# Kernel optimization log

Measured on AMD Instinct MI355X. Metric: run time of the kernel, lower is better.

The kernel has to match this reference:

```python
import jax, jax.numpy as jnp
import numpy as np
import math

THETA_BASE = 10000.0
RMS_EPS = 1.1920929e-07  # torch.finfo(float32).eps (nn.RMSNorm default eps=None)


def _rmsnorm(x, w):
    var = jnp.mean(x * x, axis=-1, keepdims=True)
    return x * jax.lax.rsqrt(var + RMS_EPS) * w


def _apply_pope(x, positions, pope_delta_raw, is_query):
    # x: (T, dk) pre-activation content -> magnitude via softplus
    dk = x.shape[-1]
    mu = jax.nn.softplus(x)
    freqs = THETA_BASE ** (jnp.arange(dk, dtype=jnp.float32) / dk)
    phi = positions[:, None] * freqs[None, :]  # (T, dk)
    if not is_query:
        phi = phi + (-2.0 * math.pi) * jax.nn.sigmoid(pope_delta_raw)
    return jnp.concatenate([mu * jnp.cos(phi), mu * jnp.sin(phi)], axis=-1)  # (T, 2*dk)


def setup_inputs() -> dict:
    key = jax.random.key(0)
    T, d, dk, dv = 8192, 1024, 64, 64
    dk_pope = 2 * dk
    ks = jax.random.split(key, 16)
    s = 0.02
    inp = {
        "x_seq": jax.random.normal(ks[0], (T, d), dtype=jnp.float32),
        "W_q": jax.random.normal(ks[1], (dk, d), dtype=jnp.float32) * s,
        "W_k": jax.random.normal(ks[2], (dk, d), dtype=jnp.float32) * s,
        "W_v": jax.random.normal(ks[3], (dv, d), dtype=jnp.float32) * s,
        "pope_delta_raw": jnp.zeros((dk,), dtype=jnp.float32),
        "W_alpha1": jax.random.normal(ks[4], (2 * dk, d), dtype=jnp.float32) * s,
        "W_alpha2": jax.random.normal(ks[5], (dk_pope, 2 * dk), dtype=jnp.float32) * s,
        "W_beta": jax.random.normal(ks[6], (1, d), dtype=jnp.float32) * s,
        "post_norm_w": jnp.ones((dv,), dtype=jnp.float32),
        "out_gate_W": jax.random.normal(ks[7], (dv, d), dtype=jnp.float32) * s,
        "W_out_W": jax.random.normal(ks[8], (d, dv), dtype=jnp.float32) * s,
        "ffn_norm_w": jnp.ones((d,), dtype=jnp.float32),
        "ffn_gate_W": jax.random.normal(ks[9], (d, d), dtype=jnp.float32) * s,
        "ffn_up_W": jax.random.normal(ks[10], (d, d), dtype=jnp.float32) * s,
        "ffn_down_W": jax.random.normal(ks[11], (d, d), dtype=jnp.float32) * s,
    }
    return inp


def reference(x_seq, W_q, W_k, W_v, pope_delta_raw, W_alpha1, W_alpha2, W_beta,
              post_norm_w, out_gate_W, W_out_W, ffn_norm_w, ffn_gate_W, ffn_up_W,
              ffn_down_W):
    T, d = x_seq.shape
    dk = W_q.shape[0]
    dk_pope = 2 * dk
    dv = W_v.shape[0]
    positions = jnp.arange(T, dtype=jnp.float32)

    q = _apply_pope(x_seq @ W_q.T, positions, pope_delta_raw, is_query=True)   # (T, dk_pope)
    k = _apply_pope(x_seq @ W_k.T, positions, pope_delta_raw, is_query=False)  # (T, dk_pope)
    v = jax.nn.silu(x_seq @ W_v.T)                                             # (T, dv)
    alpha = jax.nn.sigmoid(jax.nn.silu(x_seq @ W_alpha1.T) @ W_alpha2.T)       # (T, dk_pope)
    beta = jax.nn.sigmoid(x_seq @ W_beta.T)                                    # (T, 1)

    def step(S, inp):
        qt, kt, vt, at, bt = inp
        aS = at[:, None] * S                       # Diag(alpha) S, (dk_pope, dv)
        ktaS = kt @ aS                              # (dv,)
        S_new = aS + bt * kt[:, None] * (vt[None, :] - ktaS[None, :])
        ot = S_new.T @ qt                           # (dv,)
        return S_new, ot

    S0 = jnp.zeros((dk_pope, dv), dtype=x_seq.dtype)
    _, out = jax.lax.scan(step, S0, (q, k, v, alpha, beta))  # out: (T, dv)

    out = _rmsnorm(out, post_norm_w)
    out = out * jax.nn.sigmoid(x_seq @ out_gate_W.T)
    x = x_seq + out @ W_out_W.T
    h = _rmsnorm(x, ffn_norm_w)
    x = x + (jax.nn.silu(h @ ffn_gate_W.T) * (h @ ffn_up_W.T)) @ ffn_down_W.T
    return x
```

## Files before the change

### kernel.cpp

```cpp
#include <hip/hip_runtime.h>
#include <math.h>

#define T_SEQ 8192
#define D_MODEL 1024
#define DK 64
#define DKP 128
#define DV 64
#define C1LD 512
#define RMS_EPS 1.1920929e-07f
#define CHUNK 128
#define NCHUNK 64

typedef __attribute__((ext_vector_type(8))) __bf16 bf16x8;
typedef __attribute__((ext_vector_type(4))) float f32x4;

__device__ __forceinline__ float wave_sum(float x) {
#pragma unroll
  for (int off = 1; off < 64; off <<= 1) x += __shfl_xor(x, off, 64);
  return x;
}

template <int CTRL>
__device__ __forceinline__ float dpp_add(float x) {
  return x + __int_as_float(
                 __builtin_amdgcn_update_dpp(0, __float_as_int(x), CTRL, 0xF, 0xF, false));
}
__device__ __forceinline__ float sum16(float x) {
  x = dpp_add<0x121>(x);
  x = dpp_add<0x122>(x);
  x = dpp_add<0x124>(x);
  x = dpp_add<0x128>(x);
  return x;
}

__device__ __forceinline__ float sigmoidf_(float x) { return 1.0f / (1.0f + expf(-x)); }
__device__ __forceinline__ float siluf_(float x) { return x / (1.0f + expf(-x)); }

__device__ __forceinline__ unsigned short f2bf(float f) {
  unsigned u = __float_as_uint(f);
  u += 0x7fff + ((u >> 16) & 1);
  return (unsigned short)(u >> 16);
}

__global__ void init_tables(const float* __restrict__ delta, float* __restrict__ freq,
                            float* __restrict__ shift) {
  int i = threadIdx.x;
  freq[i] = (float)pow(10000.0, (double)i / 64.0);
  float s = 1.0f / (1.0f + expf(-delta[i]));
  shift[i] = -6.2831855f * s;
}

__global__ void build_wcat16(const float* __restrict__ Wq, const float* __restrict__ Wk,
                             const float* __restrict__ Wv, const float* __restrict__ Wa1,
                             const float* __restrict__ Wb, const float* __restrict__ Wg,
                             unsigned short* __restrict__ W16) {
  int idx = blockIdx.x * 256 + threadIdx.x;
  if (idx >= 512 * 1024) return;
  int row = idx >> 10, col = idx & 1023;
  float v = 0.f;
  if (row < 64) v = Wq[row * 1024 + col];
  else if (row < 128) v = Wk[(row - 64) * 1024 + col];
  else if (row < 192) v = Wv[(row - 128) * 1024 + col];
  else if (row < 320) v = Wa1[(row - 192) * 1024 + col];
  else if (row == 320) v = Wb[col];
  else if (row < 385) v = Wg[(row - 321) * 1024 + col];
  W16[idx] = f2bf(v);
}

__global__ void conv_bf16(const float* __restrict__ in, unsigned short* __restrict__ out,
                          int n4) {
  int i = blockIdx.x * 256 + threadIdx.x;
  if (i >= n4) return;
  float4 v = ((const float4*)in)[i];
  uint2 o;
  o.x = (unsigned)f2bf(v.x) | ((unsigned)f2bf(v.y) << 16);
  o.y = (unsigned)f2bf(v.z) | ((unsigned)f2bf(v.w) << 16);
  ((uint2*)out)[i] = o;
}

__global__ void conv_weights(const float* __restrict__ Wg, const float* __restrict__ Wu,
                             const float* __restrict__ Wd, const float* __restrict__ Wo,
                             unsigned short* __restrict__ Wg16, unsigned short* __restrict__ Wu16,
                             unsigned short* __restrict__ Wd16, unsigned short* __restrict__ Wo16) {
  int i = blockIdx.x * 256 + threadIdx.x;
  const float* src;
  unsigned short* dst;
  int base;
  if (i < 262144) { src = Wg; dst = Wg16; base = i; }
  else if (i < 524288) { src = Wu; dst = Wu16; base = i - 262144; }
  else if (i < 786432) { src = Wd; dst = Wd16; base = i - 524288; }
  else if (i < 802816) { src = Wo; dst = Wo16; base = i - 786432; }
  else return;
  float4 v = ((const float4*)src)[base];
  uint2 o;
  o.x = (unsigned)f2bf(v.x) | ((unsigned)f2bf(v.y) << 16);
  o.y = (unsigned)f2bf(v.z) | ((unsigned)f2bf(v.w) << 16);
  ((uint2*)dst)[base] = o;
}

__global__ __launch_bounds__(256) void gemm_bf16(const unsigned short* __restrict__ A,
                                                 const unsigned short* __restrict__ B,
                                                 const float* __restrict__ add,
                                                 float* __restrict__ C,
                                                 int M, int N, int K, int act) {
  __shared__ unsigned short As[128 * 32];
  __shared__ unsigned short Bs[128 * 32];
  const int tid = threadIdx.x;
  const int tm0 = blockIdx.x * 128, tn0 = blockIdx.y * 128;
  const int lane = tid & 63;
  const int w = tid >> 6;
  const int wr = (w >> 1) * 64, wc = (w & 1) * 64;
  const int fr = lane & 15, fq = lane >> 4;
  const int seg = w << 5;
  const int srow = lane >> 2;
  const int skc = (lane & 3) * 8;
  f32x4 acc[4][4];
#pragma unroll
  for (int a = 0; a < 4; ++a)
#pragma unroll
    for (int b = 0; b < 4; ++b) acc[a][b] = (f32x4){0.f, 0.f, 0.f, 0.f};

  for (int k0 = 0; k0 < K; k0 += 32) {
    __syncthreads();
#pragma unroll
    for (int j = 0; j < 2; ++j) {
      int r = seg + j * 16 + srow;
      __builtin_amdgcn_global_load_lds(
          (const __attribute__((address_space(1))) unsigned int*)(A + (size_t)(tm0 + r) * K + k0 + skc),
          (__attribute__((address_space(3))) unsigned int*)(As + (seg + j * 16) * 32),
          16, 0, 0);
      __builtin_amdgcn_global_load_lds(
          (const __attribute__((address_space(1))) unsigned int*)(B + (size_t)(tn0 + r) * K + k0 + skc),
          (__attribute__((address_space(3))) unsigned int*)(Bs + (seg + j * 16) * 32),
          16, 0, 0);
    }
    __syncthreads();
    bf16x8 af[4], bfr[4];
#pragma unroll
    for (int a = 0; a < 4; ++a)
      af[a] = *(const bf16x8*)(As + (wr + a * 16 + fr) * 32 + fq * 8);
#pragma unroll
    for (int b = 0; b < 4; ++b)
      bfr[b] = *(const bf16x8*)(Bs + (wc + b * 16 + fr) * 32 + fq * 8);
#pragma unroll
    for (int a = 0; a < 4; ++a)
#pragma unroll
      for (int b = 0; b < 4; ++b)
        acc[a][b] = __builtin_amdgcn_mfma_f32_16x16x32_bf16(af[a], bfr[b], acc[a][b], 0, 0, 0);
  }
#pragma unroll
  for (int a = 0; a < 4; ++a) {
#pragma unroll
    for (int b = 0; b < 4; ++b) {
#pragma unroll
      for (int r = 0; r < 4; ++r) {
        int row = tm0 + wr + a * 16 + fq * 4 + r;
        int col = tn0 + wc + b * 16 + fr;
        float v = acc[a][b][r];
        if (add) v += add[(size_t)row * N + col];
        if (act == 2) v = v / (1.0f + expf(-v));
        C[(size_t)row * N + col] = v;
      }
    }
  }
}

__global__ __launch_bounds__(256) void gemm_f32(const float* __restrict__ A,
                                                const float* __restrict__ B,
                                                const float* __restrict__ add,
                                                float* __restrict__ C,
                                                int M, int N, int K, int act) {
  __shared__ float As[16][68];
  __shared__ float Bs[16][68];
  const int bm = blockIdx.x * 64;
  const int bn = blockIdx.y * 64;
  const int tid = threadIdx.x;
  const int tm = tid >> 4, tn = tid & 15;
  const int lk = (tid & 3) << 2, lm = tid >> 2;
  float acc[4][4] = {{0.f}};
  const int ar = bm + lm;
  const int br = bn + lm;
  for (int k0 = 0; k0 < K; k0 += 16) {
    float4 a4 = make_float4(0.f, 0.f, 0.f, 0.f);
    float4 b4 = make_float4(0.f, 0.f, 0.f, 0.f);
    if (ar < M) a4 = *(const float4*)(A + (size_t)ar * K + k0 + lk);
    if (br < N) b4 = *(const float4*)(B + (size_t)br * K + k0 + lk);
    __syncthreads();
    As[lk][lm] = a4.x; As[lk + 1][lm] = a4.y; As[lk + 2][lm] = a4.z; As[lk + 3][lm] = a4.w;
    Bs[lk][lm] = b4.x; Bs[lk + 1][lm] = b4.y; Bs[lk + 2][lm] = b4.z; Bs[lk + 3][lm] = b4.w;
    __syncthreads();
#pragma unroll
    for (int kk = 0; kk < 16; ++kk) {
      float4 av = *(const float4*)&As[kk][tm << 2];
      float4 bv = *(const float4*)&Bs[kk][tn << 2];
      float a_[4] = {av.x, av.y, av.z, av.w};
      float b_[4] = {bv.x, bv.y, bv.z, bv.w};
#pragma unroll
      for (int i = 0; i < 4; ++i)
#pragma unroll
        for (int j = 0; j < 4; ++j) acc[i][j] = fmaf(a_[i], b_[j], acc[i][j]);
    }
  }
#pragma unroll
  for (int i = 0; i < 4; ++i) {
    int row = bm + (tm << 2) + i;
    if (row >= M) continue;
#pragma unroll
    for (int j = 0; j < 4; ++j) {
      int col = bn + (tn << 2) + j;
      if (col >= N) continue;
      float r = acc[i][j];
      if (add) r += add[(size_t)row * N + col];
      if (act == 1) r = 1.0f / (1.0f + expf(-r));
      else if (act == 2) r = r / (1.0f + expf(-r));
      C[(size_t)row * N + col] = r;
    }
  }
}

__global__ void act_split(const float* __restrict__ C1, float* __restrict__ vb,
                          float* __restrict__ a1s, float* __restrict__ betab) {
  int idx = blockIdx.x * 256 + threadIdx.x;
  if (idx >= T_SEQ * 193) return;
  int t = idx / 193, j = idx % 193;
  if (j < 64) {
    float x = C1[(size_t)t * C1LD + 128 + j];
    vb[(size_t)t * DV + j] = siluf_(x);
  } else if (j < 192) {
    float x = C1[(size_t)t * C1LD + 192 + (j - 64)];
    a1s[(size_t)t * DKP + (j - 64)] = siluf_(x);
  } else {
    betab[t] = sigmoidf_(C1[(size_t)t * C1LD + 320]);
  }
}

__global__ __launch_bounds__(256) void pope_kernel(const float* __restrict__ C1,
                                                   const float* __restrict__ freq,
                                                   const float* __restrict__ shift,
                                                   float* __restrict__ qb, float* __restrict__ kb) {
  int idx = blockIdx.x * 256 + threadIdx.x;
  if (idx >= T_SEQ * DK) return;
  int t = idx >> 6;
  int i = idx & 63;
  const double TWO_PI = 6.283185307179586476925286766559;
  const double INV_TWO_PI = 0.15915494309189533576888376337251;
  float phiq = (float)t * freq[i];
  float phik = phiq + shift[i];
  float xq = C1[(size_t)t * C1LD + i];
  float muq = xq > 15.f ? xq : log1pf(expf(xq));
  double w = (double)phiq * INV_TWO_PI;
  w -= floor(w);
  float aq = (float)(w * TWO_PI);
  qb[(size_t)t * DKP + i] = muq * cosf(aq);
  qb[(size_t)t * DKP + 64 + i] = muq * sinf(aq);
  float xk = C1[(size_t)t * C1LD + DK + i];
  float muk = xk > 15.f ? xk : log1pf(expf(xk));
  double wk = (double)phik * INV_TWO_PI;
  wk -= floor(wk);
  float ak = (float)(wk * TWO_PI);
  kb[(size_t)t * DKP + i] = muk * cosf(ak);
  kb[(size_t)t * DKP + 64 + i] = muk * sinf(ak);
}


__global__ __launch_bounds__(64) void scan_passA(const float* __restrict__ kb,
                                                 const float* __restrict__ alphab,
                                                 const float* __restrict__ vb,
                                                 const float* __restrict__ betab,
                                                 float* __restrict__ PT,
                                                 float* __restrict__ fstate) {
  const int chunk = blockIdx.x;
  const int w = blockIdx.y;
  const int l = threadIdx.x;
  const int sl = l & 15;
  const int task = w * 4 + (l >> 4);
  const bool isP = (task < 128);
  const int c = isP ? 0 : (task - 128);
  const float* kc = kb + (size_t)chunk * CHUNK * DKP + sl * 8;
  const float* ac = alphab + (size_t)chunk * CHUNK * DKP + sl * 8;
  const float* vcol = vb + (size_t)chunk * CHUNK * DV + c;
  const float* bp = betab + (size_t)chunk * CHUNK;
  float s[8];
#pragma unroll
  for (int i = 0; i < 8; ++i) s[i] = (isP && (sl * 8 + i == task)) ? 1.f : 0.f;
  float4 k0 = *(const float4*)kc, k1 = *(const float4*)(kc + 4);
  float4 a0 = *(const float4*)ac, a1 = *(const float4*)(ac + 4);
  float vt = isP ? 0.f : vcol[0];
  float bt = bp[0];
  for (int t = 0; t < CHUNK; ++t) {
    const int tn = (t + 1 < CHUNK) ? t + 1 : CHUNK - 1;
    float4 nk0 = *(const float4*)(kc + (size_t)tn * DKP);
    float4 nk1 = *(const float4*)(kc + (size_t)tn * DKP + 4);
    float4 na0 = *(const float4*)(ac + (size_t)tn * DKP);
    float4 na1 = *(const float4*)(ac + (size_t)tn * DKP + 4);
    float nv = isP ? 0.f : vcol[(size_t)tn * DV];
    float nb = bp[tn];
    s[0] *= a0.x; s[1] *= a0.y; s[2] *= a0.z; s[3] *= a0.w;
    s[4] *= a1.x; s[5] *= a1.y; s[6] *= a1.z; s[7] *= a1.w;
    float e0 = fmaf(s[1], k0.y, s[0] * k0.x);
    float e1 = fmaf(s[3], k0.w, s[2] * k0.z);
    float e2 = fmaf(s[5], k1.y, s[4] * k1.x);
    float e3 = fmaf(s[7], k1.w, s[6] * k1.z);
    float d = sum16((e0 + e1) + (e2 + e3));
    float cf = bt * (vt - d);
    s[0] = fmaf(cf, k0.x, s[0]); s[1] = fmaf(cf, k0.y, s[1]);
    s[2] = fmaf(cf, k0.z, s[2]); s[3] = fmaf(cf, k0.w, s[3]);
    s[4] = fmaf(cf, k1.x, s[4]); s[5] = fmaf(cf, k1.y, s[5]);
    s[6] = fmaf(cf, k1.z, s[6]); s[7] = fmaf(cf, k1.w, s[7]);
    k0 = nk0; k1 = nk1; a0 = na0; a1 = na1; vt = nv; bt = nb;
  }
  if (isP) {
    float* dst = PT + (size_t)chunk * 16384 + (size_t)task * 128 + sl * 8;
    *(float4*)dst = make_float4(s[0], s[1], s[2], s[3]);
    *(float4*)(dst + 4) = make_float4(s[4], s[5], s[6], s[7]);
  } else {
#pragma unroll
    for (int i = 0; i < 8; ++i)
      fstate[(size_t)chunk * 8192 + (size_t)(sl * 8 + i) * 64 + c] = s[i];
  }
}

__global__ __launch_bounds__(256) void scan_combine(const float* __restrict__ PT,
                                                    const float* __restrict__ fstate,
                                                    float* __restrict__ sinbuf) {
  const int c = blockIdx.x;
  const int r = threadIdx.x & 127;
  const int h = threadIdx.x >> 7;
  __shared__ float sv[128];
  __shared__ float part[128];
  float bufA[64], bufB[64];
  const float* Pbase = PT + (size_t)h * 64 * 128 + r;
#pragma unroll
  for (int jj = 0; jj < 64; ++jj) bufA[jj] = Pbase[(size_t)jj * 128];
  float s = 0.f;
#define COMBINE_ITER(J, CUR, NXT)                                                  \
  {                                                                                \
    if (h == 0) {                                                                  \
      sinbuf[(size_t)(J) * 8192 + (size_t)r * 64 + c] = s;                         \
      sv[r] = s;                                                                   \
    }                                                                              \
    __syncthreads();                                                               \
    int jn = ((J) + 1 < NCHUNK) ? (J) + 1 : NCHUNK - 1;                            \
    const float* Pn = Pbase + (size_t)jn * 16384;                                  \
    _Pragma("unroll")                                                              \
    for (int jj = 0; jj < 64; ++jj) NXT[jj] = Pn[(size_t)jj * 128];                \
    const float* svh = sv + h * 64;                                                \
    float a0 = (h == 0) ? fstate[(size_t)(J) * 8192 + (size_t)r * 64 + c] : 0.f;   \
    float a1 = 0.f, a2 = 0.f, a3 = 0.f;                                            \
    _Pragma("unroll")                                                              \
    for (int jj = 0; jj < 64; jj += 4) {                                           \
      a0 = fmaf(CUR[jj], svh[jj], a0);                                             \
      a1 = fmaf(CUR[jj + 1], svh[jj + 1], a1);                                     \
      a2 = fmaf(CUR[jj + 2], svh[jj + 2], a2);                                     \
      a3 = fmaf(CUR[jj + 3], svh[jj + 3], a3);                                     \
    }                                                                              \
    float tot = (a0 + a1) + (a2 + a3);                                             \
    if (h == 1) part[r] = tot;                                                     \
    __syncthreads();                                                               \
    if (h == 0) s = tot + part[r];                                                 \
  }
  for (int j = 0; j < NCHUNK; j += 2) {
    COMBINE_ITER(j, bufA, bufB)
    COMBINE_ITER(j + 1, bufB, bufA)
  }
#undef COMBINE_ITER
}

__global__ __launch_bounds__(64) void scan_passB(const float* __restrict__ qb,
                                                 const float* __restrict__ kb,
                                                 const float* __restrict__ alphab,
                                                 const float* __restrict__ vb,
                                                 const float* __restrict__ betab,
                                                 const float* __restrict__ sinbuf,
                                                 float* __restrict__ ob) {
  const int chunk = blockIdx.x;
  const int l = threadIdx.x;
  const int sl = l & 15;
  const int c = blockIdx.y * 4 + (l >> 4);
  const float* kc = kb + (size_t)chunk * CHUNK * DKP + sl * 8;
  const float* ac = alphab + (size_t)chunk * CHUNK * DKP + sl * 8;
  const float* qc = qb + (size_t)chunk * CHUNK * DKP + sl * 8;
  const float* vcol = vb + (size_t)chunk * CHUNK * DV + c;
  const float* bp = betab + (size_t)chunk * CHUNK;
  float* ocol = ob + (size_t)chunk * CHUNK * DV + c;
  float s[8];
#pragma unroll
  for (int i = 0; i < 8; ++i)
    s[i] = sinbuf[(size_t)chunk * 8192 + (size_t)(sl * 8 + i) * 64 + c];
  float4 k0 = *(const float4*)kc, k1 = *(const float4*)(kc + 4);
  float4 a0 = *(const float4*)ac, a1 = *(const float4*)(ac + 4);
  float4 q0 = *(const float4*)qc, q1 = *(const float4*)(qc + 4);
  float vt = vcol[0], bt = bp[0];
  for (int t = 0; t < CHUNK; ++t) {
    const int tn = (t + 1 < CHUNK) ? t + 1 : CHUNK - 1;
    float4 nk0 = *(const float4*)(kc + (size_t)tn * DKP);
    float4 nk1 = *(const float4*)(kc + (size_t)tn * DKP + 4);
    float4 na0 = *(const float4*)(ac + (size_t)tn * DKP);
    float4 na1 = *(const float4*)(ac + (size_t)tn * DKP + 4);
    float4 nq0 = *(const float4*)(qc + (size_t)tn * DKP);
    float4 nq1 = *(const float4*)(qc + (size_t)tn * DKP + 4);
    float nv = vcol[(size_t)tn * DV];
    float nb = bp[tn];
    s[0] *= a0.x; s[1] *= a0.y; s[2] *= a0.z; s[3] *= a0.w;
    s[4] *= a1.x; s[5] *= a1.y; s[6] *= a1.z; s[7] *= a1.w;
    float e0 = fmaf(s[1], k0.y, s[0] * k0.x);
    float e1 = fmaf(s[3], k0.w, s[2] * k0.z);
    float e2 = fmaf(s[5], k1.y, s[4] * k1.x);
    float e3 = fmaf(s[7], k1.w, s[6] * k1.z);
    float d = sum16((e0 + e1) + (e2 + e3));
    float cf = bt * (vt - d);
    s[0] = fmaf(cf, k0.x, s[0]); s[1] = fmaf(cf, k0.y, s[1]);
    s[2] = fmaf(cf, k0.z, s[2]); s[3] = fmaf(cf, k0.w, s[3]);
    s[4] = fmaf(cf, k1.x, s[4]); s[5] = fmaf(cf, k1.y, s[5]);
    s[6] = fmaf(cf, k1.z, s[6]); s[7] = fmaf(cf, k1.w, s[7]);
    float f0 = fmaf(s[1], q0.y, s[0] * q0.x);
    float f1 = fmaf(s[3], q0.w, s[2] * q0.z);
    float f2 = fmaf(s[5], q1.y, s[4] * q1.x);
    float f3 = fmaf(s[7], q1.w, s[6] * q1.z);
    float e = sum16((f0 + f1) + (f2 + f3));
    if (sl == 0) ocol[(size_t)t * DV] = e;
    k0 = nk0; k1 = nk1; a0 = na0; a1 = na1; q0 = nq0; q1 = nq1; vt = nv; bt = nb;
  }
}

__global__ __launch_bounds__(256) void post_kernel(const float* __restrict__ ob,
                                                   const float* __restrict__ C1,
                                                   const float* __restrict__ pnw,
                                                   unsigned short* __restrict__ og16) {
  int row = blockIdx.x * 4 + (threadIdx.x >> 6);
  int c = threadIdx.x & 63;
  float o = ob[(size_t)row * DV + c];
  float ss = wave_sum(o * o);
  float scale = 1.0f / sqrtf(ss * (1.0f / DV) + RMS_EPS);
  float g = sigmoidf_(C1[(size_t)row * C1LD + 321 + c]);
  og16[(size_t)row * DV + c] = f2bf(o * scale * pnw[c] * g);
}

__global__ __launch_bounds__(256) void rmsnorm_rows(const float* __restrict__ x,
                                                    const float* __restrict__ w,
                                                    unsigned short* __restrict__ y) {
  int row = blockIdx.x;
  const float4* x4 = (const float4*)(x + (size_t)row * D_MODEL);
  const float4* w4 = (const float4*)w;
  float4 v = x4[threadIdx.x];
  float ss = v.x * v.x + v.y * v.y + v.z * v.z + v.w * v.w;
  ss = wave_sum(ss);
  __shared__ float red[4];
  if ((threadIdx.x & 63) == 0) red[threadIdx.x >> 6] = ss;
  __syncthreads();
  float tot = red[0] + red[1] + red[2] + red[3];
  float scale = 1.0f / sqrtf(tot * (1.0f / D_MODEL) + RMS_EPS);
  float4 wv = w4[threadIdx.x];
  uint2 o;
  o.x = (unsigned)f2bf(v.x * scale * wv.x) | ((unsigned)f2bf(v.y * scale * wv.y) << 16);
  o.y = (unsigned)f2bf(v.z * scale * wv.z) | ((unsigned)f2bf(v.w * scale * wv.w) << 16);
  ((uint2*)(y + (size_t)row * D_MODEL))[threadIdx.x] = o;
}

__global__ void mul_to_bf16(const float* __restrict__ G, const float* __restrict__ U,
                            unsigned short* __restrict__ O, int n4) {
  int i = blockIdx.x * 256 + threadIdx.x;
  if (i >= n4) return;
  float4 g = ((const float4*)G)[i];
  float4 u = ((const float4*)U)[i];
  uint2 o;
  o.x = (unsigned)f2bf(g.x * u.x) | ((unsigned)f2bf(g.y * u.y) << 16);
  o.y = (unsigned)f2bf(g.z * u.z) | ((unsigned)f2bf(g.w * u.w) << 16);
  ((uint2*)O)[i] = o;
}

extern "C" void kernel_launch(void* const* d_in, const int* in_sizes, int n_in,
                              void* d_out, int out_size, void* d_ws, size_t ws_size,
                              hipStream_t stream) {
  const float* x_seq = (const float*)d_in[0];
  const float* W_q = (const float*)d_in[1];
  const float* W_k = (const float*)d_in[2];
  const float* W_v = (const float*)d_in[3];
  const float* pope_delta = (const float*)d_in[4];
  const float* W_a1 = (const float*)d_in[5];
  const float* W_a2 = (const float*)d_in[6];
  const float* W_beta = (const float*)d_in[7];
  const float* pnw = (const float*)d_in[8];
  const float* out_gate_W = (const float*)d_in[9];
  const float* W_out = (const float*)d_in[10];
  const float* ffn_norm_w = (const float*)d_in[11];
  const float* Wg = (const float*)d_in[12];
  const float* Wu = (const float*)d_in[13];
  const float* Wd = (const float*)d_in[14];
  float* out = (float*)d_out;

  float* F = (float*)d_ws;
  float* freq_f = F;
  float* shift_f = F + 64;
  size_t o = 256;
  unsigned short* Wcat16 = (unsigned short*)(F + o); o += 262144;
  unsigned short* Wg16   = (unsigned short*)(F + o); o += 524288;
  unsigned short* Wu16   = (unsigned short*)(F + o); o += 524288;
  unsigned short* Wd16   = (unsigned short*)(F + o); o += 524288;
  unsigned short* Wout16 = (unsigned short*)(F + o); o += 32768;
  unsigned short* og16   = (unsigned short*)(F + o); o += 262144;
  float* BIG = F + o;
  float* C1 = BIG;
  float* qb = C1 + 4194304;
  float* kb = qb + 1048576;
  float* alphab = kb + 1048576;
  float* a1s = alphab + 1048576;
  float* vb = a1s + 1048576;
  float* betab = vb + 524288;
  float* ob = betab + 8192;
  float* PT = ob + 524288;
  float* fstate = PT + 1048576;
  float* sinbuf = fstate + 524288;
  unsigned short* x16 = (unsigned short*)(sinbuf + 524288);
  unsigned short* hb16 = (unsigned short*)BIG;
  unsigned short* GU16 = (unsigned short*)BIG;
  float* Gb = BIG + 4194304;
  float* Ub = Gb + 8388608;

  (void)in_sizes; (void)n_in; (void)out_size; (void)ws_size;

  init_tables<<<1, 64, 0, stream>>>(pope_delta, freq_f, shift_f);
  build_wcat16<<<(512 * 1024 + 255) / 256, 256, 0, stream>>>(W_q, W_k, W_v, W_a1, W_beta,
                                                             out_gate_W, Wcat16);
  conv_bf16<<<(2097152 + 255) / 256, 256, 0, stream>>>(x_seq, x16, 2097152);
  conv_weights<<<(802816 + 255) / 256, 256, 0, stream>>>(Wg, Wu, Wd, W_out,
                                                         Wg16, Wu16, Wd16, Wout16);
  gemm_bf16<<<dim3(64, 4), 256, 0, stream>>>(x16, Wcat16, nullptr, C1, T_SEQ, 512, 1024, 0);
  act_split<<<(T_SEQ * 193 + 255) / 256, 256, 0, stream>>>(C1, vb, a1s, betab);
  gemm_f32<<<dim3(128, 2), 256, 0, stream>>>(a1s, W_a2, nullptr, alphab, T_SEQ, DKP, DKP, 1);
  pope_kernel<<<(T_SEQ * DK + 255) / 256, 256, 0, stream>>>(C1, freq_f, shift_f, qb, kb);
  scan_passA<<<dim3(NCHUNK, 48), 64, 0, stream>>>(kb, alphab, vb, betab, PT, fstate);
  scan_combine<<<64, 256, 0, stream>>>(PT, fstate, sinbuf);
  scan_passB<<<dim3(NCHUNK, 16), 64, 0, stream>>>(qb, kb, alphab, vb, betab, sinbuf, ob);
  post_kernel<<<T_SEQ / 4, 256, 0, stream>>>(ob, C1, pnw, og16);
  gemm_bf16<<<dim3(64, 8), 256, 0, stream>>>(og16, Wout16, x_seq, out, T_SEQ, D_MODEL, 64, 0);
  rmsnorm_rows<<<T_SEQ, 256, 0, stream>>>(out, ffn_norm_w, hb16);
  gemm_bf16<<<dim3(64, 8), 256, 0, stream>>>(hb16, Wg16, nullptr, Gb, T_SEQ, D_MODEL, D_MODEL, 2);
  gemm_bf16<<<dim3(64, 8), 256, 0, stream>>>(hb16, Wu16, nullptr, Ub, T_SEQ, D_MODEL, D_MODEL, 0);
  mul_to_bf16<<<(2097152 + 255) / 256, 256, 0, stream>>>(Gb, Ub, GU16, 2097152);
  gemm_bf16<<<dim3(64, 8), 256, 0, stream>>>(GU16, Wd16, out, out, T_SEQ, D_MODEL, D_MODEL, 0);
}
```

Measured before the change: 535.8 us.

## Widen scan combine to 1024 threads and transpose state layout for vector access

```diff
diff --git a/kernel.cpp b/kernel.cpp
--- a/kernel.cpp
+++ b/kernel.cpp
@@ -314,56 +314,101 @@
     *(float4*)dst = make_float4(s[0], s[1], s[2], s[3]);
     *(float4*)(dst + 4) = make_float4(s[4], s[5], s[6], s[7]);
   } else {
-#pragma unroll
-    for (int i = 0; i < 8; ++i)
-      fstate[(size_t)chunk * 8192 + (size_t)(sl * 8 + i) * 64 + c] = s[i];
-  }
-}
-
-__global__ __launch_bounds__(256) void scan_combine(const float* __restrict__ PT,
-                                                    const float* __restrict__ fstate,
-                                                    float* __restrict__ sinbuf) {
+    float* fd = fstate + (size_t)chunk * 8192 + (size_t)c * 128 + sl * 8;
+    *(float4*)fd = make_float4(s[0], s[1], s[2], s[3]);
+    *(float4*)(fd + 4) = make_float4(s[4], s[5], s[6], s[7]);
+  }
+}
+
+__global__ __launch_bounds__(1024) void scan_combine(const float* __restrict__ PT,
+                                                     const float* __restrict__ fstate,
+                                                     float* __restrict__ sinbuf) {
   const int c = blockIdx.x;
-  const int r = threadIdx.x & 127;
-  const int h = threadIdx.x >> 7;
+  const int tid = threadIdx.x;
+  const int r = tid & 127;
+  const int q = tid >> 7;
   __shared__ float sv[128];
-  __shared__ float part[128];
-  float bufA[64], bufB[64];
-  const float* Pbase = PT + (size_t)h * 64 * 128 + r;
-#pragma unroll
-  for (int jj = 0; jj < 64; ++jj) bufA[jj] = Pbase[(size_t)jj * 128];
+  __shared__ float part[8][128];
+  const float* Pb = PT + (size_t)q * 2048 + r;
+  float bufA[16], bufB[16];
+#pragma unroll
+  for (int i = 0; i < 16; ++i) bufA[i] = Pb[(size_t)i * 128];
   float s = 0.f;
-#define COMBINE_ITER(J, CUR, NXT)                                                  \
+#define CITER(J, CUR, NXT)                                                         \
   {                                                                                \
-    if (h == 0) {                                                                  \
-      sinbuf[(size_t)(J) * 8192 + (size_t)r * 64 + c] = s;                         \
+    float fJ = 0.f;                                                                \
+    if (q == 0) {                                                                  \
+      sinbuf[(size_t)(J) * 8192 + (size_t)c * 128 + r] = s;                        \
       sv[r] = s;                                                                   \
+      fJ = fstate[(size_t)(J) * 8192 + (size_t)c * 128 + r];                       \
     }                                                                              \
     __syncthreads();                                                               \
     int jn = ((J) + 1 < NCHUNK) ? (J) + 1 : NCHUNK - 1;                            \
-    const float* Pn = Pbase + (size_t)jn * 16384;                                  \
+    const float* Pn = Pb + (size_t)jn * 16384;                                     \
     _Pragma("unroll")                                                              \
-    for (int jj = 0; jj < 64; ++jj) NXT[jj] = Pn[(size_t)jj * 128];                \
-    const float* svh = sv + h * 64;                                                \
-    float a0 = (h == 0) ? fstate[(size_t)(J) * 8192 + (size_t)r * 64 + c] : 0.f;   \
-    float a1 = 0.f, a2 = 0.f, a3 = 0.f;                                            \
+    for (int i = 0; i < 16; ++i) NXT[i] = Pn[(size_t)i * 128];                     \
+    float a0 = 0.f, a1 = 0.f, a2 = 0.f, a3 = 0.f;                                  \
     _Pragma("unroll")                                                              \
-    for (int jj = 0; jj < 64; jj += 4) {                                           \
-      a0 = fmaf(CUR[jj], svh[jj], a0);                                             \
-      a1 = fmaf(CUR[jj + 1], svh[jj + 1], a1);                                     \
-      a2 = fmaf(CUR[jj + 2], svh[jj + 2], a2);                                     \
-      a3 = fmaf(CUR[jj + 3], svh[jj + 3], a3);                                     \
+    for (int i = 0; i < 16; i += 4) {                                              \
+      a0 = fmaf(CUR[i], sv[q * 16 + i], a0);                                       \
+      a1 = fmaf(CUR[i + 1], sv[q * 16 + i + 1], a1);                               \
+      a2 = fmaf(CUR[i + 2], sv[q * 16 + i + 2], a2);                               \
+      a3 = fmaf(CUR[i + 3], sv[q * 16 + i + 3], a3);                               \
     }                                                                              \
-    float tot = (a0 + a1) + (a2 + a3);                                             \
-    if (h == 1) part[r] = tot;                                                     \
+    part[q][r] = (a0 + a1) + (a2 + a3);                                            \
     __syncthreads();                                                               \
-    if (h == 0) s = tot + part[r];                                                 \
+    if (q == 0) {                                                                  \
+      float t8 = ((part[0][r] + part[1][r]) + (part[2][r] + part[3][r])) +         \
+                 ((part[4][r] + part[5][r]) + (part[6][r] + part[7][r]));          \
+      s = t8 + fJ;                                                                 \
+    }                                                                              \
   }
   for (int j = 0; j < NCHUNK; j += 2) {
-    COMBINE_ITER(j, bufA, bufB)
-    COMBINE_ITER(j + 1, bufB, bufA)
-  }
-#undef COMBINE_ITER
+    CITER(j, bufA, bufB)
+    CITER(j + 1, bufB, bufA)
+  }
+#undef CITER
+}
+
+struct PBIn {
+  float4 k0, k1, a0, a1, q0, q1;
+  float v, b;
+};
+
+__device__ __forceinline__ PBIn pb_load(const float* kc, const float* ac, const float* qc,
+                                        const float* vcol, const float* bp, int t) {
+  int tt = (t < CHUNK) ? t : CHUNK - 1;
+  PBIn in;
+  in.k0 = *(const float4*)(kc + (size_t)tt * DKP);
+  in.k1 = *(const float4*)(kc + (size_t)tt * DKP + 4);
+  in.a0 = *(const float4*)(ac + (size_t)tt * DKP);
+  in.a1 = *(const float4*)(ac + (size_t)tt * DKP + 4);
+  in.q0 = *(const float4*)(qc + (size_t)tt * DKP);
+  in.q1 = *(const float4*)(qc + (size_t)tt * DKP + 4);
+  in.v = vcol[(size_t)tt * DV];
+  in.b = bp[tt];
+  return in;
+}
+
+__device__ __forceinline__ void pb_step(float s[8], const PBIn& in, int sl, float* ocol, int t) {
+  s[0] *= in.a0.x; s[1] *= in.a0.y; s[2] *= in.a0.z; s[3] *= in.a0.w;
+  s[4] *= in.a1.x; s[5] *= in.a1.y; s[6] *= in.a1.z; s[7] *= in.a1.w;
+  float e0 = fmaf(s[1], in.k0.y, s[0] * in.k0.x);
+  float e1 = fmaf(s[3], in.k0.w, s[2] * in.k0.z);
+  float e2 = fmaf(s[5], in.k1.y, s[4] * in.k1.x);
+  float e3 = fmaf(s[7], in.k1.w, s[6] * in.k1.z);
+  float d = sum16((e0 + e1) + (e2 + e3));
+  float cf = in.b * (in.v - d);
+  s[0] = fmaf(cf, in.k0.x, s[0]); s[1] = fmaf(cf, in.k0.y, s[1]);
+  s[2] = fmaf(cf, in.k0.z, s[2]); s[3] = fmaf(cf, in.k0.w, s[3]);
+  s[4] = fmaf(cf, in.k1.x, s[4]); s[5] = fmaf(cf, in.k1.y, s[5]);
+  s[6] = fmaf(cf, in.k1.z, s[6]); s[7] = fmaf(cf, in.k1.w, s[7]);
+  float f0 = fmaf(s[1], in.q0.y, s[0] * in.q0.x);
+  float f1 = fmaf(s[3], in.q0.w, s[2] * in.q0.z);
+  float f2 = fmaf(s[5], in.q1.y, s[4] * in.q1.x);
+  float f3 = fmaf(s[7], in.q1.w, s[6] * in.q1.z);
+  float e = sum16((f0 + f1) + (f2 + f3));
+  if (sl == 0) ocol[(size_t)t * DV] = e;
 }
 
 __global__ __launch_bounds__(64) void scan_passB(const float* __restrict__ qb,
@@ -384,42 +429,17 @@
   const float* bp = betab + (size_t)chunk * CHUNK;
   float* ocol = ob + (size_t)chunk * CHUNK * DV + c;
   float s[8];
-#pragma unroll
-  for (int i = 0; i < 8; ++i)
-    s[i] = sinbuf[(size_t)chunk * 8192 + (size_t)(sl * 8 + i) * 64 + c];
-  float4 k0 = *(const float4*)kc, k1 = *(const float4*)(kc + 4);
-  float4 a0 = *(const float4*)ac, a1 = *(const float4*)(ac + 4);
-  float4 q0 = *(const float4*)qc, q1 = *(const float4*)(qc + 4);
-  float vt = vcol[0], bt = bp[0];
-  for (int t = 0; t < CHUNK; ++t) {
-    const int tn = (t + 1 < CHUNK) ? t + 1 : CHUNK - 1;
-    float4 nk0 = *(const float4*)(kc + (size_t)tn * DKP);
-    float4 nk1 = *(const float4*)(kc + (size_t)tn * DKP + 4);
-    float4 na0 = *(const float4*)(ac + (size_t)tn * DKP);
-    float4 na1 = *(const float4*)(ac + (size_t)tn * DKP + 4);
-    float4 nq0 = *(const float4*)(qc + (size_t)tn * DKP);
-    float4 nq1 = *(const float4*)(qc + (size_t)tn * DKP + 4);
-    float nv = vcol[(size_t)tn * DV];
-    float nb = bp[tn];
-    s[0] *= a0.x; s[1] *= a0.y; s[2] *= a0.z; s[3] *= a0.w;
-    s[4] *= a1.x; s[5] *= a1.y; s[6] *= a1.z; s[7] *= a1.w;
-    float e0 = fmaf(s[1], k0.y, s[0] * k0.x);
-    float e1 = fmaf(s[3], k0.w, s[2] * k0.z);
-    float e2 = fmaf(s[5], k1.y, s[4] * k1.x);
-    float e3 = fmaf(s[7], k1.w, s[6] * k1.z);
-    float d = sum16((e0 + e1) + (e2 + e3));
-    float cf = bt * (vt - d);
-    s[0] = fmaf(cf, k0.x, s[0]); s[1] = fmaf(cf, k0.y, s[1]);
-    s[2] = fmaf(cf, k0.z, s[2]); s[3] = fmaf(cf, k0.w, s[3]);
-    s[4] = fmaf(cf, k1.x, s[4]); s[5] = fmaf(cf, k1.y, s[5]);
-    s[6] = fmaf(cf, k1.z, s[6]); s[7] = fmaf(cf, k1.w, s[7]);
-    float f0 = fmaf(s[1], q0.y, s[0] * q0.x);
-    float f1 = fmaf(s[3], q0.w, s[2] * q0.z);
-    float f2 = fmaf(s[5], q1.y, s[4] * q1.x);
-    float f3 = fmaf(s[7], q1.w, s[6] * q1.z);
-    float e = sum16((f0 + f1) + (f2 + f3));
-    if (sl == 0) ocol[(size_t)t * DV] = e;
-    k0 = nk0; k1 = nk1; a0 = na0; a1 = na1; q0 = nq0; q1 = nq1; vt = nv; bt = nb;
+  const float* sbase = sinbuf + (size_t)chunk * 8192 + (size_t)c * 128 + sl * 8;
+  float4 si0 = *(const float4*)sbase, si1 = *(const float4*)(sbase + 4);
+  s[0] = si0.x; s[1] = si0.y; s[2] = si0.z; s[3] = si0.w;
+  s[4] = si1.x; s[5] = si1.y; s[6] = si1.z; s[7] = si1.w;
+  PBIn inA = pb_load(kc, ac, qc, vcol, bp, 0);
+  PBIn inB = pb_load(kc, ac, qc, vcol, bp, 1);
+  for (int t = 0; t < CHUNK; t += 2) {
+    pb_step(s, inA, sl, ocol, t);
+    inA = pb_load(kc, ac, qc, vcol, bp, t + 2);
+    pb_step(s, inB, sl, ocol, t + 1);
+    inB = pb_load(kc, ac, qc, vcol, bp, t + 3);
   }
 }
 
@@ -530,7 +550,7 @@
   gemm_f32<<<dim3(128, 2), 256, 0, stream>>>(a1s, W_a2, nullptr, alphab, T_SEQ, DKP, DKP, 1);
   pope_kernel<<<(T_SEQ * DK + 255) / 256, 256, 0, stream>>>(C1, freq_f, shift_f, qb, kb);
   scan_passA<<<dim3(NCHUNK, 48), 64, 0, stream>>>(kb, alphab, vb, betab, PT, fstate);
-  scan_combine<<<64, 256, 0, stream>>>(PT, fstate, sinbuf);
+  scan_combine<<<64, 1024, 0, stream>>>(PT, fstate, sinbuf);
   scan_passB<<<dim3(NCHUNK, 16), 64, 0, stream>>>(qb, kb, alphab, vb, betab, sinbuf, ob);
   post_kernel<<<T_SEQ / 4, 256, 0, stream>>>(ob, C1, pnw, og16);
   gemm_bf16<<<dim3(64, 8), 256, 0, stream>>>(og16, Wout16, x_seq, out, T_SEQ, D_MODEL, 64, 0);
```

Result: slower. 623.9 us (+16.5%).

## Widen scan_combine to 1024 threads and transpose state buffers for coalescing

Applied to the files above, without the earlier changes.

```diff
diff --git a/kernel.cpp b/kernel.cpp
--- a/kernel.cpp
+++ b/kernel.cpp
@@ -314,56 +314,60 @@
     *(float4*)dst = make_float4(s[0], s[1], s[2], s[3]);
     *(float4*)(dst + 4) = make_float4(s[4], s[5], s[6], s[7]);
   } else {
-#pragma unroll
-    for (int i = 0; i < 8; ++i)
-      fstate[(size_t)chunk * 8192 + (size_t)(sl * 8 + i) * 64 + c] = s[i];
-  }
-}
-
-__global__ __launch_bounds__(256) void scan_combine(const float* __restrict__ PT,
-                                                    const float* __restrict__ fstate,
-                                                    float* __restrict__ sinbuf) {
+    float* fd = fstate + (size_t)chunk * 8192 + (size_t)c * 128 + sl * 8;
+    *(float4*)fd = make_float4(s[0], s[1], s[2], s[3]);
+    *(float4*)(fd + 4) = make_float4(s[4], s[5], s[6], s[7]);
+  }
+}
+
+__global__ __launch_bounds__(1024) void scan_combine(const float* __restrict__ PT,
+                                                     const float* __restrict__ fstate,
+                                                     float* __restrict__ sinbuf) {
   const int c = blockIdx.x;
-  const int r = threadIdx.x & 127;
-  const int h = threadIdx.x >> 7;
+  const int tid = threadIdx.x;
+  const int r = tid & 127;
+  const int q = tid >> 7;
   __shared__ float sv[128];
-  __shared__ float part[128];
-  float bufA[64], bufB[64];
-  const float* Pbase = PT + (size_t)h * 64 * 128 + r;
-#pragma unroll
-  for (int jj = 0; jj < 64; ++jj) bufA[jj] = Pbase[(size_t)jj * 128];
+  __shared__ float part[8][128];
+  const float* Pb = PT + (size_t)q * 2048 + r;
+  float bufA[16], bufB[16];
+#pragma unroll
+  for (int i = 0; i < 16; ++i) bufA[i] = Pb[(size_t)i * 128];
   float s = 0.f;
-#define COMBINE_ITER(J, CUR, NXT)                                                  \
+#define CITER(J, CUR, NXT)                                                         \
   {                                                                                \
-    if (h == 0) {                                                                  \
-      sinbuf[(size_t)(J) * 8192 + (size_t)r * 64 + c] = s;                         \
+    float fJ = 0.f;                                                                \
+    if (q == 0) {                                                                  \
+      sinbuf[(size_t)(J) * 8192 + (size_t)c * 128 + r] = s;                        \
       sv[r] = s;                                                                   \
+      fJ = fstate[(size_t)(J) * 8192 + (size_t)c * 128 + r];                       \
     }                                                                              \
     __syncthreads();                                                               \
     int jn = ((J) + 1 < NCHUNK) ? (J) + 1 : NCHUNK - 1;                            \
-    const float* Pn = Pbase + (size_t)jn * 16384;                                  \
+    const float* Pn = Pb + (size_t)jn * 16384;                                     \
     _Pragma("unroll")                                                              \
-    for (int jj = 0; jj < 64; ++jj) NXT[jj] = Pn[(size_t)jj * 128];                \
-    const float* svh = sv + h * 64;                                                \
-    float a0 = (h == 0) ? fstate[(size_t)(J) * 8192 + (size_t)r * 64 + c] : 0.f;   \
-    float a1 = 0.f, a2 = 0.f, a3 = 0.f;                                            \
+    for (int i = 0; i < 16; ++i) NXT[i] = Pn[(size_t)i * 128];                     \
+    float a0 = 0.f, a1 = 0.f, a2 = 0.f, a3 = 0.f;                                  \
     _Pragma("unroll")                                                              \
-    for (int jj = 0; jj < 64; jj += 4) {                                           \
-      a0 = fmaf(CUR[jj], svh[jj], a0);                                             \
-      a1 = fmaf(CUR[jj + 1], svh[jj + 1], a1);                                     \
-      a2 = fmaf(CUR[jj + 2], svh[jj + 2], a2);                                     \
-      a3 = fmaf(CUR[jj + 3], svh[jj + 3], a3);                                     \
+    for (int i = 0; i < 16; i += 4) {                                              \
+      a0 = fmaf(CUR[i], sv[q * 16 + i], a0);                                       \
+      a1 = fmaf(CUR[i + 1], sv[q * 16 + i + 1], a1);                               \
+      a2 = fmaf(CUR[i + 2], sv[q * 16 + i + 2], a2);                               \
+      a3 = fmaf(CUR[i + 3], sv[q * 16 + i + 3], a3);                               \
     }                                                                              \
-    float tot = (a0 + a1) + (a2 + a3);                                             \
-    if (h == 1) part[r] = tot;                                                     \
+    part[q][r] = (a0 + a1) + (a2 + a3);                                            \
     __syncthreads();                                                               \
-    if (h == 0) s = tot + part[r];                                                 \
+    if (q == 0) {                                                                  \
+      float t8 = ((part[0][r] + part[1][r]) + (part[2][r] + part[3][r])) +         \
+                 ((part[4][r] + part[5][r]) + (part[6][r] + part[7][r]));          \
+      s = t8 + fJ;                                                                 \
+    }                                                                              \
   }
   for (int j = 0; j < NCHUNK; j += 2) {
-    COMBINE_ITER(j, bufA, bufB)
-    COMBINE_ITER(j + 1, bufB, bufA)
-  }
-#undef COMBINE_ITER
+    CITER(j, bufA, bufB)
+    CITER(j + 1, bufB, bufA)
+  }
+#undef CITER
 }
 
 __global__ __launch_bounds__(64) void scan_passB(const float* __restrict__ qb,
@@ -384,9 +388,10 @@
   const float* bp = betab + (size_t)chunk * CHUNK;
   float* ocol = ob + (size_t)chunk * CHUNK * DV + c;
   float s[8];
-#pragma unroll
-  for (int i = 0; i < 8; ++i)
-    s[i] = sinbuf[(size_t)chunk * 8192 + (size_t)(sl * 8 + i) * 64 + c];
+  const float* sbase = sinbuf + (size_t)chunk * 8192 + (size_t)c * 128 + sl * 8;
+  float4 si0 = *(const float4*)sbase, si1 = *(const float4*)(sbase + 4);
+  s[0] = si0.x; s[1] = si0.y; s[2] = si0.z; s[3] = si0.w;
+  s[4] = si1.x; s[5] = si1.y; s[6] = si1.z; s[7] = si1.w;
   float4 k0 = *(const float4*)kc, k1 = *(const float4*)(kc + 4);
   float4 a0 = *(const float4*)ac, a1 = *(const float4*)(ac + 4);
   float4 q0 = *(const float4*)qc, q1 = *(const float4*)(qc + 4);
@@ -530,7 +535,7 @@
   gemm_f32<<<dim3(128, 2), 256, 0, stream>>>(a1s, W_a2, nullptr, alphab, T_SEQ, DKP, DKP, 1);
   pope_kernel<<<(T_SEQ * DK + 255) / 256, 256, 0, stream>>>(C1, freq_f, shift_f, qb, kb);
   scan_passA<<<dim3(NCHUNK, 48), 64, 0, stream>>>(kb, alphab, vb, betab, PT, fstate);
-  scan_combine<<<64, 256, 0, stream>>>(PT, fstate, sinbuf);
+  scan_combine<<<64, 1024, 0, stream>>>(PT, fstate, sinbuf);
   scan_passB<<<dim3(NCHUNK, 16), 64, 0, stream>>>(qb, kb, alphab, vb, betab, sinbuf, ob);
   post_kernel<<<T_SEQ / 4, 256, 0, stream>>>(ob, C1, pnw, og16);
   gemm_bf16<<<dim3(64, 8), 256, 0, stream>>>(og16, Wout16, x_seq, out, T_SEQ, D_MODEL, 64, 0);
```

Result: faster. 495.9 us (-7.4%).
